# Kernel tuning notes

Measured on AMD Instinct MI355X. Metric: run time of the kernel, lower is better.

Reference implementation:

```python
import jax, jax.numpy as jnp
import numpy as np

B, S, D = 1, 4096, 2048
H, KVH, HD = 16, 2, 128  # heads, kv heads, head_dim
GROUPS = H // KVH
ROPE_THETA = 1e6


def rotate_half(x):
    x1, x2 = x[..., : HD // 2], x[..., HD // 2:]
    return jnp.concatenate((-x2, x1), axis=-1)


def setup_inputs() -> dict:
    key = jax.random.key(0)
    ks = jax.random.split(key, 8)
    std = 0.02
    return {
        "hidden_states": jax.random.normal(ks[0], (B, S, D), jnp.float32),
        "position_ids": jnp.arange(S, dtype=jnp.int64 if jax.config.jax_enable_x64 else jnp.int32)[None, :].repeat(B, 0),
        "Wq": jax.random.normal(ks[1], (D, H * HD), jnp.float32) * std,
        "bq": jax.random.normal(ks[2], (H * HD,), jnp.float32) * std,
        "Wk": jax.random.normal(ks[3], (D, KVH * HD), jnp.float32) * std,
        "bk": jax.random.normal(ks[4], (KVH * HD,), jnp.float32) * std,
        "Wv": jax.random.normal(ks[5], (D, KVH * HD), jnp.float32) * std,
        "bv": jax.random.normal(ks[6], (KVH * HD,), jnp.float32) * std,
        "Wo": jax.random.normal(ks[7], (H * HD, D), jnp.float32) * std,
    }


def reference(hidden_states, position_ids, Wq, bq, Wk, bk, Wv, bv, Wo):
    bsz, q_len, _ = hidden_states.shape
    # projections (W stored as [in, out], equivalent to torch Linear weight.T)
    q = (hidden_states @ Wq + bq).reshape(bsz, q_len, H, HD).transpose(0, 2, 1, 3)
    k = (hidden_states @ Wk + bk).reshape(bsz, q_len, KVH, HD).transpose(0, 2, 1, 3)
    v = (hidden_states @ Wv + bv).reshape(bsz, q_len, KVH, HD).transpose(0, 2, 1, 3)

    # rotary embedding cache
    inv_freq = 1.0 / (ROPE_THETA ** (jnp.arange(0, HD, 2, dtype=jnp.float32) / HD))
    t = jnp.arange(q_len, dtype=jnp.float32)
    freqs = jnp.outer(t, inv_freq)                       # [S, HD/2]
    emb = jnp.concatenate((freqs, freqs), axis=-1)       # [S, HD]
    cos = jnp.cos(emb)[position_ids][:, None]            # [B,1,S,HD]
    sin = jnp.sin(emb)[position_ids][:, None]

    q = q * cos + rotate_half(q) * sin
    k = k * cos + rotate_half(k) * sin

    # GQA: expand kv heads (repeat_interleave along head dim)
    k = jnp.repeat(k, GROUPS, axis=1)                    # [B,H,S,HD]
    v = jnp.repeat(v, GROUPS, axis=1)

    scores = jnp.einsum("bhqd,bhkd->bhqk", q, k) / np.sqrt(HD)
    attn = jax.nn.softmax(scores.astype(jnp.float32), axis=-1).astype(q.dtype)
    out = jnp.einsum("bhqk,bhkd->bhqd", attn, v)         # [B,H,S,HD]
    out = out.transpose(0, 2, 1, 3).reshape(bsz, q_len, H * HD)
    return out @ Wo
```

## Files before the change

kernel.cpp:

```cpp
#include <hip/hip_runtime.h>

typedef unsigned short ushort_t;
typedef unsigned int u32;
typedef __attribute__((ext_vector_type(8))) short bf16x8;
typedef __attribute__((ext_vector_type(4))) float f32x4;
typedef __attribute__((ext_vector_type(16))) float f32x16;
typedef __attribute__((ext_vector_type(4))) unsigned int u32x4;

#define AS3(p) ((__attribute__((address_space(3))) unsigned int*)(p))
#define AS1(p) ((const __attribute__((address_space(1))) unsigned int*)(p))

__device__ __forceinline__ void gl_lds16(const void* g, void* l) {
  __builtin_amdgcn_global_load_lds(AS1(g), AS3(l), 16, 0, 0);
}

__device__ __forceinline__ ushort_t f2bf(float f) {
  unsigned u = __float_as_uint(f);
  u += 0x7FFFu + ((u >> 16) & 1u);
  return (ushort_t)(u >> 16);
}

__device__ __forceinline__ float bf2f(u32 hi16) { return __uint_as_float(hi16 << 16); }

__device__ __forceinline__ u32 cvtpk(float a, float b) {
  u32 r;
  asm("v_cvt_pk_bf16_f32 %0, %1, %2" : "=v"(r) : "v"(a), "v"(b));
  return r;
}


__global__ void k_rope(const int* __restrict__ pid, float2* __restrict__ tab) {
  int t = blockIdx.x * 256 + threadIdx.x;
  int s = t >> 6, j = t & 63;
  double inv = pow(1000000.0, -(double)j / 64.0);
  double a = (double)pid[s] * inv;
  tab[t] = make_float2((float)cos(a), (float)sin(a));
}

__global__ void k_cvt(const float* __restrict__ in, unsigned char* __restrict__ out) {
  int i = blockIdx.x * 256 + threadIdx.x;
  float4 v = ((const float4*)in)[i];
  ushort_t r[4] = { f2bf(v.x), f2bf(v.y), f2bf(v.z), f2bf(v.w) };
  *(ulonglong1*)(out + (size_t)i * 8) = *(ulonglong1*)r;
}

__global__ void k_transpose(const float* __restrict__ W, unsigned char* __restrict__ outT, int N) {
  __shared__ float tile[32][33];
  int n0 = blockIdx.x * 32, k0 = blockIdx.y * 32;
  int tx = threadIdx.x & 31, ty = threadIdx.x >> 5;
  #pragma unroll
  for (int i = 0; i < 4; ++i)
    tile[ty + i * 8][tx] = W[(size_t)(k0 + ty + i * 8) * N + n0 + tx];
  __syncthreads();
  #pragma unroll
  for (int i = 0; i < 4; ++i) {
    int n = ty + i * 8;
    *(ushort_t*)(outT + ((size_t)(n0 + n) * 2048 + k0 + tx) * 2) = f2bf(tile[tx][n]);
  }
}

__device__ __forceinline__ void gemm_loop(
    const unsigned char* __restrict__ aSrc0,
    const unsigned char* __restrict__ bSrc0,
    unsigned char* ldsA, unsigned char* ldsB,
    f32x4 acc[2][8])
{
  const int tid = threadIdx.x;
  const int lane = tid & 63, wave = tid >> 6;
  const int c = lane & 15, g = lane >> 4;

  int rowS[4], swzS[4];
  #pragma unroll
  for (int i = 0; i < 4; ++i) {
    int o = (i * 4 + wave) * 1024 + lane * 16;
    int row = o >> 7, slot = (o >> 4) & 7;
    rowS[i] = row;
    swzS[i] = (slot ^ (row & 7)) << 4;
  }
  #pragma unroll
  for (int mi = 0; mi < 2; ++mi)
    for (int nj = 0; nj < 8; ++nj)
      for (int q = 0; q < 4; ++q) acc[mi][nj][q] = 0.0f;

  for (int kt = 0; kt < 32; ++kt) {
    __syncthreads();
    #pragma unroll
    for (int i = 0; i < 4; ++i) {
      gl_lds16(aSrc0 + (size_t)rowS[i] * 4096 + kt * 128 + swzS[i], ldsA + (i * 4 + wave) * 1024);
      gl_lds16(bSrc0 + (size_t)rowS[i] * 4096 + kt * 128 + swzS[i], ldsB + (i * 4 + wave) * 1024);
    }
    __syncthreads();
    #pragma unroll
    for (int ks = 0; ks < 2; ++ks) {
      bf16x8 a[2];
      #pragma unroll
      for (int mi = 0; mi < 2; ++mi) {
        int row = wave * 32 + mi * 16 + c;
        a[mi] = *(const bf16x8*)(ldsA + row * 128 + (((ks * 4 + g) ^ (row & 7)) << 4));
      }
      #pragma unroll
      for (int nj = 0; nj < 8; ++nj) {
        int row = nj * 16 + c;
        bf16x8 b = *(const bf16x8*)(ldsB + row * 128 + (((ks * 4 + g) ^ (row & 7)) << 4));
        acc[0][nj] = __builtin_amdgcn_mfma_f32_16x16x32_bf16(a[0], b, acc[0][nj], 0, 0, 0);
        acc[1][nj] = __builtin_amdgcn_mfma_f32_16x16x32_bf16(a[1], b, acc[1][nj], 0, 0, 0);
      }
    }
  }
}


__global__ __launch_bounds__(256, 2) void k_qkv_gemm(
    const unsigned char* __restrict__ hidB, const unsigned char* __restrict__ wT,
    const float* __restrict__ bq, const float* __restrict__ bk, const float* __restrict__ bv,
    const float2* __restrict__ rope,
    unsigned char* __restrict__ Qs, unsigned char* __restrict__ Ks, unsigned char* __restrict__ VTs)
{
  __shared__ alignas(16) unsigned char lds[32768];
  const int bx = blockIdx.x;
  const int swz = (bx & 7) * 80 + (bx >> 3);
  const int bm = swz / 20, bn = swz % 20;
  f32x4 acc[2][8];
  gemm_loop(hidB + (size_t)bm * 128 * 4096, wT + (size_t)bn * 128 * 4096, lds, lds + 16384, acc);

  const int lane = threadIdx.x & 63, wave = threadIdx.x >> 6;
  const int c = lane & 15, g = lane >> 4;
  const int n0 = bn * 128;
  float bias[8];
  #pragma unroll
  for (int nj = 0; nj < 8; ++nj) {
    int n = n0 + nj * 16 + c;
    bias[nj] = (n < 2048) ? bq[n] : (n < 2304 ? bk[n - 2048] : bv[n - 2304]);
  }
  const int m0 = bm * 128 + wave * 32;
  if (n0 < 2304) {
    constexpr float SCALE_Q = 0.08838834764831845f * 1.4426950408889634f;
    const bool isQ = (n0 < 2048);
    unsigned char* out = isQ ? (Qs + (size_t)(n0 >> 7) * 4096 * 256)
                             : (Ks + (size_t)((n0 - 2048) >> 7) * 4096 * 256);
    const float scl = isQ ? SCALE_Q : 1.0f;
    #pragma unroll
    for (int mi = 0; mi < 2; ++mi)
      #pragma unroll
      for (int r = 0; r < 4; ++r) {
        int srow = m0 + mi * 16 + g * 4 + r;
        #pragma unroll
        for (int nj = 0; nj < 4; ++nj) {
          int d = nj * 16 + c;
          float2 cs = rope[srow * 64 + d];
          float x1 = acc[mi][nj][r] + bias[nj];
          float x2 = acc[mi][nj + 4][r] + bias[nj + 4];
          float o1 = (x1 * cs.x - x2 * cs.y) * scl;
          float o2 = (x2 * cs.x + x1 * cs.y) * scl;
          *(ushort_t*)(out + (size_t)srow * 256 + d * 2) = f2bf(o1);
          *(ushort_t*)(out + (size_t)srow * 256 + (d + 64) * 2) = f2bf(o2);
        }
      }
  } else {
    unsigned char* out = VTs + (size_t)((n0 - 2304) >> 7) * 128 * 8192;
    #pragma unroll
    for (int mi = 0; mi < 2; ++mi)
      #pragma unroll
      for (int r = 0; r < 4; ++r) {
        int srow = m0 + mi * 16 + g * 4 + r;
        #pragma unroll
        for (int nj = 0; nj < 8; ++nj) {
          int d = nj * 16 + c;
          *(ushort_t*)(out + (size_t)d * 8192 + srow * 2) = f2bf(acc[mi][nj][r] + bias[nj]);
        }
      }
  }
}


__global__ __launch_bounds__(256, 3) void k_attn(
    const unsigned char* __restrict__ Qs, const unsigned char* __restrict__ Ks,
    const unsigned char* __restrict__ VTs,
    unsigned char* __restrict__ P0, unsigned char* __restrict__ P1,
    float* __restrict__ L0, float* __restrict__ L1)
{
  __shared__ alignas(16) unsigned char lds[32768];
  const int tid = threadIdx.x, lane = tid & 63, wave = tid >> 6;
  const int l31 = lane & 31, hi = lane >> 5;
  const int qt = blockIdx.x, h = blockIdx.y, sp = blockIdx.z, kvh = h >> 3;

  bf16x8 qv[8];
  const unsigned char* qbase = Qs + ((size_t)h * 4096 + qt * 128 + wave * 32 + l31) * 256;
  #pragma unroll
  for (int dks = 0; dks < 8; ++dks)
    qv[dks] = *(const bf16x8*)(qbase + dks * 32 + hi * 16);

  f32x16 o[4];
  #pragma unroll
  for (int dn = 0; dn < 4; ++dn)
    #pragma unroll
    for (int r = 0; r < 16; ++r) o[dn][r] = 0.0f;
  float lsum = 0.0f;

  const unsigned char* kbase = Ks + (size_t)kvh * 4096 * 256 + (size_t)sp * 2048 * 256;
  const unsigned char* vbase = VTs + (size_t)kvh * 128 * 8192 + (size_t)sp * 2048 * 2;

  int kOff[2]; size_t vOff[2];
  #pragma unroll
  for (int i = 0; i < 2; ++i) {
    int o_ = (i * 4 + wave) * 1024 + lane * 16;
    int row = o_ >> 8, slot = (o_ >> 4) & 15;
    int sw = slot ^ (row & 15);
    kOff[i] = row * 256 + sw * 16;
    int d = ((sw >> 2) << 5) + row;
    vOff[i] = (size_t)d * 8192 + (sw & 3) * 16;
  }

  auto STAGE = [&](int t, int b) {
    const unsigned char* kst = kbase + (size_t)t * 8192;
    const unsigned char* vst = vbase + (size_t)t * 64;
    unsigned char* dK = lds + b * 8192;
    unsigned char* dV = lds + 16384 + b * 8192;
    #pragma unroll
    for (int i = 0; i < 2; ++i) {
      gl_lds16(kst + kOff[i], dK + (i * 4 + wave) * 1024);
      gl_lds16(vst + vOff[i], dV + (i * 4 + wave) * 1024);
    }
  };

  STAGE(0, 0);
  __syncthreads();

  for (int t = 0; t < 64; ++t) {
    const int cur = t & 1;
    if (t < 63) STAGE(t + 1, cur ^ 1);

    const unsigned char* Kb = lds + cur * 8192;
    const unsigned char* Vb = lds + 16384 + cur * 8192;

    f32x16 sA;
    #pragma unroll
    for (int r = 0; r < 16; ++r) sA[r] = 0.0f;
    __builtin_amdgcn_s_setprio(1);
    #pragma unroll
    for (int dks = 0; dks < 8; ++dks) {
      bf16x8 k0 = *(const bf16x8*)(Kb + l31 * 256 + ((((dks << 1) | hi) ^ (l31 & 15)) << 4));
      sA = __builtin_amdgcn_mfma_f32_32x32x16_bf16(k0, qv[dks], sA, 0, 0, 0);
    }
    __builtin_amdgcn_s_setprio(0);

    #pragma unroll
    for (int r = 0; r < 16; ++r) sA[r] = exp2f(sA[r]);
    float t0 = (sA[0] + sA[1]) + (sA[2] + sA[3]);
    float t1 = (sA[4] + sA[5]) + (sA[6] + sA[7]);
    float t2 = (sA[8] + sA[9]) + (sA[10] + sA[11]);
    float t3 = (sA[12] + sA[13]) + (sA[14] + sA[15]);
    lsum += (t0 + t1) + (t2 + t3);

    bf16x8 pa[2];
    #pragma unroll
    for (int part = 0; part < 2; ++part) {
      int base = part * 8;
      u32 A0 = cvtpk(sA[base + 0], sA[base + 1]);
      u32 A1 = cvtpk(sA[base + 2], sA[base + 3]);
      u32 B0 = cvtpk(sA[base + 4], sA[base + 5]);
      u32 B1 = cvtpk(sA[base + 6], sA[base + 7]);
      asm volatile("v_permlane32_swap_b32 %0, %1" : "+v"(A0), "+v"(B0));
      asm volatile("v_permlane32_swap_b32 %0, %1" : "+v"(A1), "+v"(B1));
      union { u32x4 u; bf16x8 b; } cv;
      cv.u = (u32x4){A0, A1, B0, B1};
      pa[part] = cv.b;
    }

    __builtin_amdgcn_s_setprio(1);
    #pragma unroll
    for (int ks4 = 0; ks4 < 2; ++ks4) {
      #pragma unroll
      for (int dn = 0; dn < 4; ++dn) {
        int slotIdx = (dn << 2) | (ks4 << 1) | hi;
        bf16x8 vf = *(const bf16x8*)(Vb + l31 * 256 + ((slotIdx ^ (l31 & 15)) << 4));
        o[dn] = __builtin_amdgcn_mfma_f32_32x32x16_bf16(pa[ks4], vf, o[dn], 0, 0, 0);
      }
    }
    __builtin_amdgcn_s_setprio(0);

    __syncthreads();
  }

  lsum += __shfl_xor(lsum, 32);
  float inv = 1.0f / lsum;
  unsigned char* P = sp ? P1 : P0;
  #pragma unroll
  for (int r = 0; r < 16; ++r) {
    int crow = (r & 3) + 8 * (r >> 2) + 4 * hi;
    float invq = __shfl(inv, (lane & 32) | crow);
    int srow = qt * 128 + wave * 32 + crow;
    #pragma unroll
    for (int dn = 0; dn < 4; ++dn)
      *(ushort_t*)(P + ((size_t)srow * 2048 + h * 128 + dn * 32 + l31) * 2) =
          f2bf(o[dn][r] * invq);
  }
  if (hi == 0) {
    float* L = sp ? L1 : L0;
    L[h * 4096 + qt * 128 + wave * 32 + l31] = lsum;
  }
}


__global__ void k_comb(unsigned char* __restrict__ P0, const unsigned char* __restrict__ P1,
                       const float* __restrict__ L0, const float* __restrict__ L1)
{
  int g = blockIdx.x * 256 + threadIdx.x;
  u32x4 a = *(const u32x4*)(P0 + (size_t)g * 16);
  u32x4 b = *(const u32x4*)(P1 + (size_t)g * 16);
  int e0 = g * 8;
  int srow = e0 >> 11, hh = (e0 >> 7) & 15;
  float l0 = L0[hh * 4096 + srow], l1 = L1[hh * 4096 + srow];
  float inv = 1.0f / (l0 + l1);
  float w0 = l0 * inv, w1 = l1 * inv;
  ushort_t r[8];
  #pragma unroll
  for (int j = 0; j < 4; ++j) {
    float lo = bf2f(a[j] & 0xFFFFu) * w0 + bf2f(b[j] & 0xFFFFu) * w1;
    float hi2 = bf2f(a[j] >> 16) * w0 + bf2f(b[j] >> 16) * w1;
    r[2 * j] = f2bf(lo);
    r[2 * j + 1] = f2bf(hi2);
  }
  *(u32x4*)(P0 + (size_t)g * 16) = *(u32x4*)r;
}


__global__ __launch_bounds__(256, 2) void k_out_gemm(
    const unsigned char* __restrict__ AO, const unsigned char* __restrict__ woT,
    float* __restrict__ out)
{
  __shared__ alignas(16) unsigned char lds[32768];
  const int bx = blockIdx.x;
  const int swz = (bx & 7) * 64 + (bx >> 3);
  const int bm = swz >> 4, bn = swz & 15;
  f32x4 acc[2][8];
  gemm_loop(AO + (size_t)bm * 128 * 4096, woT + (size_t)bn * 128 * 4096, lds, lds + 16384, acc);
  const int lane = threadIdx.x & 63, wave = threadIdx.x >> 6;
  const int c = lane & 15, g = lane >> 4;
  const int m0 = bm * 128 + wave * 32;
  #pragma unroll
  for (int mi = 0; mi < 2; ++mi)
    #pragma unroll
    for (int r = 0; r < 4; ++r) {
      int row = m0 + mi * 16 + g * 4 + r;
      #pragma unroll
      for (int nj = 0; nj < 8; ++nj)
        out[(size_t)row * 2048 + bn * 128 + nj * 16 + c] = acc[mi][nj][r];
    }
}


extern "C" void kernel_launch(void* const* d_in, const int* in_sizes, int n_in,
                              void* d_out, int out_size, void* d_ws, size_t ws_size,
                              hipStream_t stream) {
  const float* hidden = (const float*)d_in[0];
  const int*   pos    = (const int*)d_in[1];
  const float* Wq = (const float*)d_in[2];
  const float* bq = (const float*)d_in[3];
  const float* Wk = (const float*)d_in[4];
  const float* bk = (const float*)d_in[5];
  const float* Wv = (const float*)d_in[6];
  const float* bv = (const float*)d_in[7];
  const float* Wo = (const float*)d_in[8];
  float* out = (float*)d_out;
  unsigned char* ws = (unsigned char*)d_ws;

  float2*        rope  = (float2*)(ws + 0);
  unsigned char* hidB  = ws + 2097152;
  unsigned char* woT   = ws + 18874368;
  unsigned char* Qs    = ws + 27262976;
  unsigned char* Ks    = ws + 44040192;
  unsigned char* VTs   = ws + 46137344;
  float*         L0    = (float*)(ws + 48234496);
  float*         L1    = (float*)(ws + 48496640);
  unsigned char* wqkvT = ws + 48758784;
  unsigned char* P1    = ws + 48758784;
  unsigned char* P0    = hidB;

  k_rope<<<1024, 256, 0, stream>>>(pos, rope);
  k_cvt<<<8192, 256, 0, stream>>>(hidden, hidB);
  k_transpose<<<dim3(64, 64), 256, 0, stream>>>(Wq, wqkvT, 2048);
  k_transpose<<<dim3(8, 64), 256, 0, stream>>>(Wk, wqkvT + (size_t)2048 * 2048 * 2, 256);
  k_transpose<<<dim3(8, 64), 256, 0, stream>>>(Wv, wqkvT + (size_t)2304 * 2048 * 2, 256);
  k_transpose<<<dim3(64, 64), 256, 0, stream>>>(Wo, woT, 2048);
  k_qkv_gemm<<<640, 256, 0, stream>>>(hidB, wqkvT, bq, bk, bv, rope, Qs, Ks, VTs);
  k_attn<<<dim3(32, 16, 2), 256, 0, stream>>>(Qs, Ks, VTs, P0, P1, L0, L1);
  k_comb<<<4096, 256, 0, stream>>>(P0, P1, L0, L1);
  k_out_gemm<<<512, 256, 0, stream>>>(P0, woT, out);
}
```

Measured before the change: 285.9 us.

## Software-pipeline QK^T one tile ahead of softmax and PV in attention loop

```diff
diff --git a/kernel.cpp b/kernel.cpp
--- a/kernel.cpp
+++ b/kernel.cpp
@@ -9,6 +9,12 @@
 
 #define AS3(p) ((__attribute__((address_space(3))) unsigned int*)(p))
 #define AS1(p) ((const __attribute__((address_space(1))) unsigned int*)(p))
+
+#if __has_builtin(__builtin_amdgcn_exp2f)
+#define EXP2(x) __builtin_amdgcn_exp2f(x)
+#else
+#define EXP2(x) exp2f(x)
+#endif
 
 __device__ __forceinline__ void gl_lds16(const void* g, void* l) {
   __builtin_amdgcn_global_load_lds(AS1(g), AS3(l), 16, 0, 0);
@@ -211,55 +217,64 @@
     vOff[i] = (size_t)d * 8192 + (sw & 3) * 16;
   }
 
-  auto STAGE = [&](int t, int b) {
+  auto STAGE_K = [&](int t, int b) {
     const unsigned char* kst = kbase + (size_t)t * 8192;
+    unsigned char* dK = lds + b * 8192;
+    #pragma unroll
+    for (int i = 0; i < 2; ++i)
+      gl_lds16(kst + kOff[i], dK + (i * 4 + wave) * 1024);
+  };
+  auto STAGE_V = [&](int t, int b) {
     const unsigned char* vst = vbase + (size_t)t * 64;
-    unsigned char* dK = lds + b * 8192;
     unsigned char* dV = lds + 16384 + b * 8192;
     #pragma unroll
-    for (int i = 0; i < 2; ++i) {
-      gl_lds16(kst + kOff[i], dK + (i * 4 + wave) * 1024);
+    for (int i = 0; i < 2; ++i)
       gl_lds16(vst + vOff[i], dV + (i * 4 + wave) * 1024);
-    }
   };
 
-  STAGE(0, 0);
-  __syncthreads();
-
-  for (int t = 0; t < 64; ++t) {
-    const int cur = t & 1;
-    if (t < 63) STAGE(t + 1, cur ^ 1);
-
-    const unsigned char* Kb = lds + cur * 8192;
-    const unsigned char* Vb = lds + 16384 + cur * 8192;
-
-    f32x16 sA;
-    #pragma unroll
-    for (int r = 0; r < 16; ++r) sA[r] = 0.0f;
-    __builtin_amdgcn_s_setprio(1);
+  auto QKT = [&](int t, f32x16& SN) {
+    const unsigned char* Kb = lds + (t & 1) * 8192;
+    #pragma unroll
+    for (int r = 0; r < 16; ++r) SN[r] = 0.0f;
     #pragma unroll
     for (int dks = 0; dks < 8; ++dks) {
       bf16x8 k0 = *(const bf16x8*)(Kb + l31 * 256 + ((((dks << 1) | hi) ^ (l31 & 15)) << 4));
-      sA = __builtin_amdgcn_mfma_f32_32x32x16_bf16(k0, qv[dks], sA, 0, 0, 0);
-    }
+      SN = __builtin_amdgcn_mfma_f32_32x32x16_bf16(k0, qv[dks], SN, 0, 0, 0);
+    }
+  };
+
+  STAGE_K(0, 0);
+  STAGE_V(0, 0);
+  __syncthreads();
+  STAGE_K(1, 1);
+  f32x16 sEven, sOdd;
+  QKT(0, sEven);
+  __syncthreads();
+
+  auto ITER = [&](int t, f32x16& SC, f32x16& SN) {
+    if (t < 62) STAGE_K(t + 2, t & 1);
+    if (t < 63) STAGE_V(t + 1, (t + 1) & 1);
+
+    __builtin_amdgcn_s_setprio(1);
+    if (t < 63) QKT(t + 1, SN);
     __builtin_amdgcn_s_setprio(0);
 
     #pragma unroll
-    for (int r = 0; r < 16; ++r) sA[r] = exp2f(sA[r]);
-    float t0 = (sA[0] + sA[1]) + (sA[2] + sA[3]);
-    float t1 = (sA[4] + sA[5]) + (sA[6] + sA[7]);
-    float t2 = (sA[8] + sA[9]) + (sA[10] + sA[11]);
-    float t3 = (sA[12] + sA[13]) + (sA[14] + sA[15]);
+    for (int r = 0; r < 16; ++r) SC[r] = EXP2(SC[r]);
+    float t0 = (SC[0] + SC[1]) + (SC[2] + SC[3]);
+    float t1 = (SC[4] + SC[5]) + (SC[6] + SC[7]);
+    float t2 = (SC[8] + SC[9]) + (SC[10] + SC[11]);
+    float t3 = (SC[12] + SC[13]) + (SC[14] + SC[15]);
     lsum += (t0 + t1) + (t2 + t3);
 
     bf16x8 pa[2];
     #pragma unroll
     for (int part = 0; part < 2; ++part) {
       int base = part * 8;
-      u32 A0 = cvtpk(sA[base + 0], sA[base + 1]);
-      u32 A1 = cvtpk(sA[base + 2], sA[base + 3]);
-      u32 B0 = cvtpk(sA[base + 4], sA[base + 5]);
-      u32 B1 = cvtpk(sA[base + 6], sA[base + 7]);
+      u32 A0 = cvtpk(SC[base + 0], SC[base + 1]);
+      u32 A1 = cvtpk(SC[base + 2], SC[base + 3]);
+      u32 B0 = cvtpk(SC[base + 4], SC[base + 5]);
+      u32 B1 = cvtpk(SC[base + 6], SC[base + 7]);
       asm volatile("v_permlane32_swap_b32 %0, %1" : "+v"(A0), "+v"(B0));
       asm volatile("v_permlane32_swap_b32 %0, %1" : "+v"(A1), "+v"(B1));
       union { u32x4 u; bf16x8 b; } cv;
@@ -267,6 +282,7 @@
       pa[part] = cv.b;
     }
 
+    const unsigned char* Vb = lds + 16384 + (t & 1) * 8192;
     __builtin_amdgcn_s_setprio(1);
     #pragma unroll
     for (int ks4 = 0; ks4 < 2; ++ks4) {
@@ -280,6 +296,11 @@
     __builtin_amdgcn_s_setprio(0);
 
     __syncthreads();
+  };
+
+  for (int tt = 0; tt < 64; tt += 2) {
+    ITER(tt, sEven, sOdd);
+    ITER(tt + 1, sOdd, sEven);
   }
 
   lsum += __shfl_xor(lsum, 32);
```

Result: slower. 329.8 us (+15.4%).
